# Performance work log

Measured on AMD Instinct MI355X. Metric: run time of the kernel, lower is better.

Reference implementation:

```python
import jax, jax.numpy as jnp
import numpy as np

N_NODES = 100_000
N_EDGES = 1_600_000
N_FEAT = 64
E_FEAT = 32
OUT_FEAT = 64


def _xavier_normal(key, shape, gain):
    fan_out, fan_in = shape
    std = gain * np.sqrt(2.0 / (fan_in + fan_out))
    return jax.random.normal(key, shape, dtype=jnp.float32) * std


def setup_inputs() -> dict:
    key = jax.random.key(0)
    ks = jax.random.split(key, 9)
    d_cat = 2 * N_FEAT + E_FEAT  # 160
    n_feat = jax.random.normal(ks[0], (N_NODES, N_FEAT), dtype=jnp.float32)
    e_feat = jax.random.normal(ks[1], (N_EDGES, E_FEAT), dtype=jnp.float32)
    src = jax.random.randint(ks[2], (N_EDGES,), 0, N_NODES, dtype=jnp.int32)
    dst = jax.random.randint(ks[3], (N_EDGES,), 0, N_NODES, dtype=jnp.int32)
    gain = np.sqrt(2.0)
    bound_msg = 1.0 / np.sqrt(d_cat)
    return {
        "n_feat": n_feat,
        "e_feat": e_feat,
        "src": src,
        "dst": dst,
        # W_msg uses default torch Linear init (kaiming-uniform-ish); exact init irrelevant for correctness
        "W_msg_w": jax.random.uniform(ks[4], (OUT_FEAT, d_cat), jnp.float32, -bound_msg, bound_msg),
        "W_msg_b": jax.random.uniform(ks[5], (OUT_FEAT,), jnp.float32, -bound_msg, bound_msg),
        # W uses xavier_normal with gain sqrt(2)
        "W_w": _xavier_normal(ks[6], (2 * OUT_FEAT, d_cat), gain),
        "W_b": jax.random.uniform(ks[7], (2 * OUT_FEAT,), jnp.float32, -bound_msg, bound_msg),
        "a": _xavier_normal(ks[8], (2 * OUT_FEAT, 1), gain),
    }


def reference(n_feat, e_feat, src, dst, W_msg_w, W_msg_b, W_w, W_b, a):
    # gather: per-edge concat [E, 2*n_feat + e_feat]
    feat_cat = jnp.concatenate([n_feat[src], n_feat[dst], e_feat], axis=1)
    # edge attention logits: leaky_relu((feat_cat @ W^T + b) @ a)  -> [E]
    w_feat = feat_cat @ W_w.T + W_b                      # [E, 2*out_feat]
    logits = jax.nn.leaky_relu(w_feat @ a[:, 0])         # [E]
    # edge softmax grouped by destination node
    seg_max = jax.ops.segment_max(logits, dst, num_segments=N_NODES)  # [N]
    ex = jnp.exp(logits - seg_max[dst])                  # [E]
    seg_sum = jax.ops.segment_sum(ex, dst, num_segments=N_NODES)     # [N]
    att = ex / seg_sum[dst]                              # [E]
    # messages and weighted scatter-sum aggregation
    msg = feat_cat @ W_msg_w.T + W_msg_b                 # [E, out_feat]
    agg = jax.ops.segment_sum(att[:, None] * msg, dst, num_segments=N_NODES)  # [N, out_feat]
    return jax.nn.relu(agg)
```

## Files before the change

kernel.cpp:

```cpp
#include <hip/hip_runtime.h>
#include <hip/hip_bf16.h>
#include <hip/hip_fp16.h>

#define N_NODES 100000
#define N_EDGES 1600000
#define NF 64
#define EF 32

#define SCAN_B 512
#define SCAN_NB ((N_NODES + SCAN_B - 1) / SCAN_B)


__device__ __forceinline__ unsigned pkh2(float a, float b) {
  __half2 h = __floats2half2_rn(a, b);
  return *reinterpret_cast<unsigned*>(&h);
}

__global__ __launch_bounds__(256) void k0_prep(
    const float* __restrict__ Ww, const float* __restrict__ Wb,
    const float* __restrict__ a, const float* __restrict__ Wmsg,
    float* __restrict__ v, float* __restrict__ W1T, float* __restrict__ W2T,
    float* __restrict__ WmeT) {
  int t = threadIdx.x;
  for (int j = t; j < 160; j += 256) {
    float s = 0.f;
    for (int k = 0; k < 128; ++k) s = fmaf(a[k], Ww[k * 160 + j], s);
    v[j] = s;
  }
  if (t == 0) {
    float s = 0.f;
    for (int k = 0; k < 128; ++k) s = fmaf(a[k], Wb[k], s);
    v[160] = s;
  }
  for (int idx = t; idx < 64 * 64; idx += 256) {
    int j = idx >> 6, i = idx & 63;
    W1T[idx] = Wmsg[i * 160 + j];
    W2T[idx] = Wmsg[i * 160 + 64 + j];
  }
  for (int idx = t; idx < 32 * 64; idx += 256) {
    int j = idx >> 6, i = idx & 63;
    WmeT[idx] = Wmsg[i * 160 + 128 + j];
  }
}

__global__ __launch_bounds__(256) void k1_node(
    const float* __restrict__ nf_g, const float* __restrict__ v,
    const float* __restrict__ W1T, const float* __restrict__ W2T,
    float* __restrict__ s1, float* __restrict__ s2,
    __half* __restrict__ m_src_h, float* __restrict__ m_dst) {
  int n = blockIdx.x * 256 + threadIdx.x;
  if (n >= N_NODES) return;
  const float4* nf4 = (const float4*)(nf_g + (size_t)n * NF);
  float acc[64];
#pragma unroll
  for (int i = 0; i < 64; ++i) acc[i] = 0.f;
  float s1a = 0.f, s2a = 0.f;
  for (int j4 = 0; j4 < 16; ++j4) {
    float4 q = nf4[j4];
    float xs[4] = {q.x, q.y, q.z, q.w};
#pragma unroll
    for (int u = 0; u < 4; ++u) {
      int j = j4 * 4 + u;
      float x = xs[u];
      s1a = fmaf(v[j], x, s1a);
      s2a = fmaf(v[64 + j], x, s2a);
      const float* w = W1T + j * 64;
#pragma unroll
      for (int i = 0; i < 64; ++i) acc[i] = fmaf(w[i], x, acc[i]);
    }
  }
  s1[n] = s1a;
  s2[n] = s2a;
  uint4* ms4 = (uint4*)(m_src_h + (size_t)n * NF);
#pragma unroll
  for (int b = 0; b < 8; ++b)
    ms4[b] = make_uint4(pkh2(acc[b * 8 + 0], acc[b * 8 + 1]),
                        pkh2(acc[b * 8 + 2], acc[b * 8 + 3]),
                        pkh2(acc[b * 8 + 4], acc[b * 8 + 5]),
                        pkh2(acc[b * 8 + 6], acc[b * 8 + 7]));
#pragma unroll
  for (int i = 0; i < 64; ++i) acc[i] = 0.f;
  for (int j4 = 0; j4 < 16; ++j4) {
    float4 q = nf4[j4];
    float xs[4] = {q.x, q.y, q.z, q.w};
#pragma unroll
    for (int u = 0; u < 4; ++u) {
      int j = j4 * 4 + u;
      float x = xs[u];
      const float* w = W2T + j * 64;
#pragma unroll
      for (int i = 0; i < 64; ++i) acc[i] = fmaf(w[i], x, acc[i]);
    }
  }
  float* md = m_dst + (size_t)n * NF;
#pragma unroll
  for (int i = 0; i < 64; ++i) md[i] = acc[i];
}

__global__ __launch_bounds__(256) void k_count(const int* __restrict__ dst,
                                               int* __restrict__ cnt) {
  int e = blockIdx.x * 256 + threadIdx.x;
  if (e < N_EDGES) atomicAdd(&cnt[dst[e]], 1);
}

__global__ __launch_bounds__(SCAN_B) void kS1(const int* __restrict__ cnt,
                                              int* __restrict__ bsum) {
  __shared__ int sh[SCAN_B];
  int t = threadIdx.x;
  int i = blockIdx.x * SCAN_B + t;
  sh[t] = (i < N_NODES) ? cnt[i] : 0;
  __syncthreads();
  for (int d = SCAN_B / 2; d > 0; d >>= 1) {
    if (t < d) sh[t] += sh[t + d];
    __syncthreads();
  }
  if (t == 0) bsum[blockIdx.x] = sh[0];
}

__global__ __launch_bounds__(256) void kS2(const int* __restrict__ bsum,
                                           int* __restrict__ boff,
                                           int* __restrict__ row_ptr) {
  __shared__ int sh[256];
  int t = threadIdx.x;
  sh[t] = (t < SCAN_NB) ? bsum[t] : 0;
  __syncthreads();
  for (int d = 1; d < 256; d <<= 1) {
    int val = (t >= d) ? sh[t - d] : 0;
    __syncthreads();
    sh[t] += val;
    __syncthreads();
  }
  if (t < SCAN_NB) boff[t] = (t == 0) ? 0 : sh[t - 1];
  if (t == 255) row_ptr[N_NODES] = sh[255];
}

__global__ __launch_bounds__(SCAN_B) void kS3(const int* __restrict__ cnt,
                                              const int* __restrict__ boff,
                                              int* __restrict__ row_ptr,
                                              int* __restrict__ cursor) {
  __shared__ int sh[SCAN_B];
  int t = threadIdx.x;
  int i = blockIdx.x * SCAN_B + t;
  int val = (i < N_NODES) ? cnt[i] : 0;
  sh[t] = val;
  __syncthreads();
  for (int d = 1; d < SCAN_B; d <<= 1) {
    int u = (t >= d) ? sh[t - d] : 0;
    __syncthreads();
    sh[t] += u;
    __syncthreads();
  }
  if (i < N_NODES) {
    int excl = boff[blockIdx.x] + sh[t] - val;
    row_ptr[i] = excl;
    cursor[i] = excl;
  }
}

__global__ __launch_bounds__(256) void kE_scatter(
    const int* __restrict__ src, const int* __restrict__ dst,
    const float* __restrict__ e_feat, const float* __restrict__ s1,
    const float* __restrict__ s2, const float* __restrict__ v,
    int* __restrict__ cursor, unsigned long long* __restrict__ edata,
    __half* __restrict__ ef_s) {
  int e = blockIdx.x * 256 + threadIdx.x;
  if (e >= N_EDGES) return;
  int sn = src[e], dn = dst[e];
  const float4* efr = (const float4*)(e_feat + (size_t)e * EF);
  float4 q[8];
#pragma unroll
  for (int i = 0; i < 8; ++i) q[i] = efr[i];
  float t = 0.f;
#pragma unroll
  for (int i = 0; i < 8; ++i) {
    t = fmaf(q[i].x, v[128 + i * 4 + 0], t);
    t = fmaf(q[i].y, v[128 + i * 4 + 1], t);
    t = fmaf(q[i].z, v[128 + i * 4 + 2], t);
    t = fmaf(q[i].w, v[128 + i * 4 + 3], t);
  }
  float lg = s1[sn] + s2[dn] + t + v[160];
  float l = lg > 0.f ? lg : 0.01f * lg;
  float ex = __expf(l);
  int p = atomicAdd(&cursor[dn], 1);
  edata[p] = ((unsigned long long)(unsigned)sn << 32) |
             (unsigned long long)__float_as_uint(ex);
  uint4* o4 = (uint4*)(ef_s + (size_t)p * EF);
#pragma unroll
  for (int i = 0; i < 4; ++i)
    o4[i] = make_uint4(pkh2(q[2 * i].x, q[2 * i].y),
                       pkh2(q[2 * i].z, q[2 * i].w),
                       pkh2(q[2 * i + 1].x, q[2 * i + 1].y),
                       pkh2(q[2 * i + 1].z, q[2 * i + 1].w));
}

__global__ __launch_bounds__(256) void k3_agg(
    const int* __restrict__ row_ptr, const int2* __restrict__ edata,
    const __half* __restrict__ ef_s, const __half* __restrict__ m_src_h,
    const float* __restrict__ m_dst, const float* __restrict__ WmeT,
    const float* __restrict__ Wmsg_b, float* __restrict__ out) {
  int lane = threadIdx.x & 63;
  int wid = threadIdx.x >> 6;
  int n = blockIdx.x * 4 + wid;
  if (n >= N_NODES) return;
  int start = row_ptr[n];
  int end = row_ptr[n + 1];
  int g = lane >> 4;
  int c2 = lane & 15;
  float sum_ex = 0.f, acc_ms = 0.f;
  float aefx = 0.f, aefy = 0.f;
  for (int base = start; base < end; base += 64) {
    int2 md = make_int2(0, 0);
    if (base + lane < end) md = edata[base + lane];
    int m = end - base;
    if (m > 64) m = 64;
    int mm4 = (m + 3) & ~3;
    for (int k = 0; k < mm4; k += 4) {
      float ex0 = __uint_as_float((unsigned)__shfl(md.x, k + 0));
      float ex1 = __uint_as_float((unsigned)__shfl(md.x, k + 1));
      float ex2 = __uint_as_float((unsigned)__shfl(md.x, k + 2));
      float ex3 = __uint_as_float((unsigned)__shfl(md.x, k + 3));
      int s0 = __shfl(md.y, k + 0);
      int s1i = __shfl(md.y, k + 1);
      int s2i = __shfl(md.y, k + 2);
      int s3 = __shfl(md.y, k + 3);
      float exg = (g == 0) ? ex0 : (g == 1) ? ex1 : (g == 2) ? ex2 : ex3;
      const __half2* ep =
          (const __half2*)(ef_s + ((size_t)(base + k + g)) * EF + c2 * 2);
      float2 ef2 = __half22float2(*ep);
      aefx = fmaf(exg, ef2.x, aefx);
      aefy = fmaf(exg, ef2.y, aefy);
      float ms0 = __half2float(m_src_h[(size_t)s0 * NF + lane]);
      float ms1 = __half2float(m_src_h[(size_t)s1i * NF + lane]);
      float ms2 = __half2float(m_src_h[(size_t)s2i * NF + lane]);
      float ms3 = __half2float(m_src_h[(size_t)s3 * NF + lane]);
      sum_ex += (ex0 + ex1) + (ex2 + ex3);
      acc_ms = fmaf(ex0, ms0, acc_ms);
      acc_ms = fmaf(ex1, ms1, acc_ms);
      acc_ms = fmaf(ex2, ms2, acc_ms);
      acc_ms = fmaf(ex3, ms3, acc_ms);
    }
  }
  aefx += __shfl_xor(aefx, 16);
  aefx += __shfl_xor(aefx, 32);
  aefy += __shfl_xor(aefy, 16);
  aefy += __shfl_xor(aefy, 32);
  float mm = 0.f;
#pragma unroll
  for (int jp = 0; jp < 16; ++jp) {
    float ea = __shfl(aefx, jp);
    float eb = __shfl(aefy, jp);
    mm = fmaf(WmeT[(2 * jp) * 64 + lane], ea, mm);
    mm = fmaf(WmeT[(2 * jp + 1) * 64 + lane], eb, mm);
  }
  float o = 0.f;
  if (sum_ex > 0.f) {
    o = (acc_ms + mm) / sum_ex + m_dst[(size_t)n * NF + lane] + Wmsg_b[lane];
    o = fmaxf(o, 0.f);
  }
  out[(size_t)n * NF + lane] = o;
}

extern "C" void kernel_launch(void* const* d_in, const int* in_sizes, int n_in,
                              void* d_out, int out_size, void* d_ws,
                              size_t ws_size, hipStream_t stream) {
  const float* n_feat = (const float*)d_in[0];
  const float* e_feat = (const float*)d_in[1];
  const int* src = (const int*)d_in[2];
  const int* dst = (const int*)d_in[3];
  const float* Wmsg_w = (const float*)d_in[4];
  const float* Wmsg_b = (const float*)d_in[5];
  const float* W_w = (const float*)d_in[6];
  const float* W_b = (const float*)d_in[7];
  const float* a = (const float*)d_in[8];
  float* out = (float*)d_out;

  char* ws = (char*)d_ws;
  size_t off = 0;
  auto alloc = [&](size_t bytes) -> char* {
    char* p = ws + off;
    off = (off + bytes + 255) & ~(size_t)255;
    return p;
  };
  float* v = (float*)alloc(161 * 4);
  float* W1T = (float*)alloc(64 * 64 * 4);
  float* W2T = (float*)alloc(64 * 64 * 4);
  float* WmeT = (float*)alloc(32 * 64 * 4);
  float* s1 = (float*)alloc(N_NODES * 4);
  float* s2 = (float*)alloc(N_NODES * 4);
  __half* m_src_h = (__half*)alloc((size_t)N_NODES * NF * 2);
  float* m_dst = (float*)alloc((size_t)N_NODES * NF * 4);
  int* cnt = (int*)alloc(N_NODES * 4);
  int* row_ptr = (int*)alloc((N_NODES + 1) * 4);
  int* cursor = (int*)alloc(N_NODES * 4);
  int* bsum = (int*)alloc(SCAN_NB * 4);
  int* boff = (int*)alloc(SCAN_NB * 4);
  unsigned long long* edata = (unsigned long long*)alloc((size_t)N_EDGES * 8);
  __half* ef_s = (__half*)alloc(((size_t)N_EDGES + 8) * EF * 2);
  if (off > ws_size) return;

  k0_prep<<<1, 256, 0, stream>>>(W_w, W_b, a, Wmsg_w, v, W1T, W2T, WmeT);
  k1_node<<<(N_NODES + 255) / 256, 256, 0, stream>>>(n_feat, v, W1T, W2T, s1,
                                                     s2, m_src_h, m_dst);
  hipMemsetAsync(cnt, 0, N_NODES * 4, stream);
  k_count<<<(N_EDGES + 255) / 256, 256, 0, stream>>>(dst, cnt);
  kS1<<<SCAN_NB, SCAN_B, 0, stream>>>(cnt, bsum);
  kS2<<<1, 256, 0, stream>>>(bsum, boff, row_ptr);
  kS3<<<SCAN_NB, SCAN_B, 0, stream>>>(cnt, boff, row_ptr, cursor);
  kE_scatter<<<(N_EDGES + 255) / 256, 256, 0, stream>>>(src, dst, e_feat, s1,
                                                        s2, v, cursor, edata,
                                                        ef_s);
  k3_agg<<<(N_NODES + 3) / 4, 256, 0, stream>>>(row_ptr, (const int2*)edata,
                                                ef_s, m_src_h, m_dst, WmeT,
                                                Wmsg_b, out);
}
```

Baseline: 627.5 us.

## Embed source indices in fp16 edge-feature LSBs and compute logits in aggregation

The scatter kernel no longer computes attention logits or writes a separate 8-byte edge-data array. Instead it hides the 17-bit source node index in the low mantissa bits of the packed fp16 edge features. The aggregation kernel recovers the indices with ballots and recomputes the logit and exp from the fp16 features, s1, s2 and v. It also prefetches the next group of edges one iteration ahead. This removes an edge-sized write and read pass, at the cost of perturbing the feature LSBs and computing logits from reduced-precision features.

```diff
diff --git a/kernel.cpp b/kernel.cpp
--- a/kernel.cpp
+++ b/kernel.cpp
@@ -159,43 +159,38 @@
 
 __global__ __launch_bounds__(256) void kE_scatter(
     const int* __restrict__ src, const int* __restrict__ dst,
-    const float* __restrict__ e_feat, const float* __restrict__ s1,
-    const float* __restrict__ s2, const float* __restrict__ v,
-    int* __restrict__ cursor, unsigned long long* __restrict__ edata,
-    __half* __restrict__ ef_s) {
+    const float* __restrict__ e_feat, int* __restrict__ cursor,
+    uint4* __restrict__ ef_s4) {
   int e = blockIdx.x * 256 + threadIdx.x;
   if (e >= N_EDGES) return;
-  int sn = src[e], dn = dst[e];
+  unsigned sn = (unsigned)src[e];
+  int dn = dst[e];
+  int p = atomicAdd(&cursor[dn], 1);
   const float4* efr = (const float4*)(e_feat + (size_t)e * EF);
   float4 q[8];
 #pragma unroll
   for (int i = 0; i < 8; ++i) q[i] = efr[i];
-  float t = 0.f;
+  unsigned u[16];
 #pragma unroll
   for (int i = 0; i < 8; ++i) {
-    t = fmaf(q[i].x, v[128 + i * 4 + 0], t);
-    t = fmaf(q[i].y, v[128 + i * 4 + 1], t);
-    t = fmaf(q[i].z, v[128 + i * 4 + 2], t);
-    t = fmaf(q[i].w, v[128 + i * 4 + 3], t);
-  }
-  float lg = s1[sn] + s2[dn] + t + v[160];
-  float l = lg > 0.f ? lg : 0.01f * lg;
-  float ex = __expf(l);
-  int p = atomicAdd(&cursor[dn], 1);
-  edata[p] = ((unsigned long long)(unsigned)sn << 32) |
-             (unsigned long long)__float_as_uint(ex);
-  uint4* o4 = (uint4*)(ef_s + (size_t)p * EF);
-#pragma unroll
-  for (int i = 0; i < 4; ++i)
-    o4[i] = make_uint4(pkh2(q[2 * i].x, q[2 * i].y),
-                       pkh2(q[2 * i].z, q[2 * i].w),
-                       pkh2(q[2 * i + 1].x, q[2 * i + 1].y),
-                       pkh2(q[2 * i + 1].z, q[2 * i + 1].w));
+    u[2 * i] = pkh2(q[i].x, q[i].y);
+    u[2 * i + 1] = pkh2(q[i].z, q[i].w);
+  }
+#pragma unroll
+  for (int j = 0; j < 16; ++j)
+    u[j] = (u[j] & ~1u) | ((sn >> j) & 1u);
+  u[0] = (u[0] & ~0x10000u) | (((sn >> 16) & 1u) << 16);
+  uint4* o = ef_s4 + (size_t)p * 4;
+  o[0] = make_uint4(u[0], u[1], u[2], u[3]);
+  o[1] = make_uint4(u[4], u[5], u[6], u[7]);
+  o[2] = make_uint4(u[8], u[9], u[10], u[11]);
+  o[3] = make_uint4(u[12], u[13], u[14], u[15]);
 }
 
 __global__ __launch_bounds__(256) void k3_agg(
-    const int* __restrict__ row_ptr, const int2* __restrict__ edata,
-    const __half* __restrict__ ef_s, const __half* __restrict__ m_src_h,
+    const int* __restrict__ row_ptr, const unsigned* __restrict__ efu,
+    const __half* __restrict__ m_src_h, const float* __restrict__ s1,
+    const float* __restrict__ s2, const float* __restrict__ v,
     const float* __restrict__ m_dst, const float* __restrict__ WmeT,
     const float* __restrict__ Wmsg_b, float* __restrict__ out) {
   int lane = threadIdx.x & 63;
@@ -206,39 +201,55 @@
   int end = row_ptr[n + 1];
   int g = lane >> 4;
   int c2 = lane & 15;
+  float vlo = v[128 + 2 * c2];
+  float vhi = v[128 + 2 * c2 + 1];
+  float cbias = v[160];
+  float s2n = s2[n];
   float sum_ex = 0.f, acc_ms = 0.f;
   float aefx = 0.f, aefy = 0.f;
-  for (int base = start; base < end; base += 64) {
-    int2 md = make_int2(0, 0);
-    if (base + lane < end) md = edata[base + lane];
-    int m = end - base;
-    if (m > 64) m = 64;
-    int mm4 = (m + 3) & ~3;
-    for (int k = 0; k < mm4; k += 4) {
-      float ex0 = __uint_as_float((unsigned)__shfl(md.x, k + 0));
-      float ex1 = __uint_as_float((unsigned)__shfl(md.x, k + 1));
-      float ex2 = __uint_as_float((unsigned)__shfl(md.x, k + 2));
-      float ex3 = __uint_as_float((unsigned)__shfl(md.x, k + 3));
-      int s0 = __shfl(md.y, k + 0);
-      int s1i = __shfl(md.y, k + 1);
-      int s2i = __shfl(md.y, k + 2);
-      int s3 = __shfl(md.y, k + 3);
-      float exg = (g == 0) ? ex0 : (g == 1) ? ex1 : (g == 2) ? ex2 : ex3;
-      const __half2* ep =
-          (const __half2*)(ef_s + ((size_t)(base + k + g)) * EF + c2 * 2);
-      float2 ef2 = __half22float2(*ep);
-      aefx = fmaf(exg, ef2.x, aefx);
-      aefy = fmaf(exg, ef2.y, aefy);
-      float ms0 = __half2float(m_src_h[(size_t)s0 * NF + lane]);
-      float ms1 = __half2float(m_src_h[(size_t)s1i * NF + lane]);
-      float ms2 = __half2float(m_src_h[(size_t)s2i * NF + lane]);
-      float ms3 = __half2float(m_src_h[(size_t)s3 * NF + lane]);
-      sum_ex += (ex0 + ex1) + (ex2 + ex3);
-      acc_ms = fmaf(ex0, ms0, acc_ms);
-      acc_ms = fmaf(ex1, ms1, acc_ms);
-      acc_ms = fmaf(ex2, ms2, acc_ms);
-      acc_ms = fmaf(ex3, ms3, acc_ms);
-    }
+  int slot0 = start + g;
+  unsigned ucur = efu[(size_t)min(slot0, N_EDGES - 1) * 16 + c2];
+  for (int k = start; k < end; k += 4) {
+    int slotn = k + 4 + g;
+    unsigned unext = efu[(size_t)min(slotn, N_EDGES - 1) * 16 + c2];
+    unsigned long long b0 = __ballot((int)(ucur & 1u));
+    unsigned long long b1 = __ballot((int)(ucur & 0x10000u));
+    int s0 = (int)((b0 >> 0) & 0xFFFF) | ((int)((b1 >> 0) & 1) << 16);
+    int s1i = (int)((b0 >> 16) & 0xFFFF) | ((int)((b1 >> 16) & 1) << 16);
+    int s2i = (int)((b0 >> 32) & 0xFFFF) | ((int)((b1 >> 32) & 1) << 16);
+    int s3 = (int)((b0 >> 48) & 0xFFFF) | ((int)((b1 >> 48) & 1) << 16);
+    s0 = min(s0, N_NODES - 1);
+    s1i = min(s1i, N_NODES - 1);
+    s2i = min(s2i, N_NODES - 1);
+    s3 = min(s3, N_NODES - 1);
+    int sg = (g < 2) ? (g ? s1i : s0) : ((g == 2) ? s2i : s3);
+    float ms0 = __half2float(m_src_h[(size_t)s0 * NF + lane]);
+    float ms1 = __half2float(m_src_h[(size_t)s1i * NF + lane]);
+    float ms2 = __half2float(m_src_h[(size_t)s2i * NF + lane]);
+    float ms3 = __half2float(m_src_h[(size_t)s3 * NF + lane]);
+    __half2 h2 = *reinterpret_cast<__half2*>(&ucur);
+    float2 ef2 = __half22float2(h2);
+    float pt = fmaf(ef2.y, vhi, ef2.x * vlo);
+    pt += __shfl_xor(pt, 1);
+    pt += __shfl_xor(pt, 2);
+    pt += __shfl_xor(pt, 4);
+    pt += __shfl_xor(pt, 8);
+    float lg = s1[sg] + s2n + pt + cbias;
+    float l = lg > 0.f ? lg : 0.01f * lg;
+    float ex = __expf(l);
+    float exv = ((k + g) < end) ? ex : 0.f;
+    aefx = fmaf(exv, ef2.x, aefx);
+    aefy = fmaf(exv, ef2.y, aefy);
+    float ex0 = __shfl(exv, 0);
+    float ex1 = __shfl(exv, 16);
+    float ex2 = __shfl(exv, 32);
+    float ex3 = __shfl(exv, 48);
+    sum_ex += (ex0 + ex1) + (ex2 + ex3);
+    acc_ms = fmaf(ex0, ms0, acc_ms);
+    acc_ms = fmaf(ex1, ms1, acc_ms);
+    acc_ms = fmaf(ex2, ms2, acc_ms);
+    acc_ms = fmaf(ex3, ms3, acc_ms);
+    ucur = unext;
   }
   aefx += __shfl_xor(aefx, 16);
   aefx += __shfl_xor(aefx, 32);
@@ -294,7 +305,6 @@
   int* cursor = (int*)alloc(N_NODES * 4);
   int* bsum = (int*)alloc(SCAN_NB * 4);
   int* boff = (int*)alloc(SCAN_NB * 4);
-  unsigned long long* edata = (unsigned long long*)alloc((size_t)N_EDGES * 8);
   __half* ef_s = (__half*)alloc(((size_t)N_EDGES + 8) * EF * 2);
   if (off > ws_size) return;
 
@@ -306,10 +316,9 @@
   kS1<<<SCAN_NB, SCAN_B, 0, stream>>>(cnt, bsum);
   kS2<<<1, 256, 0, stream>>>(bsum, boff, row_ptr);
   kS3<<<SCAN_NB, SCAN_B, 0, stream>>>(cnt, boff, row_ptr, cursor);
-  kE_scatter<<<(N_EDGES + 255) / 256, 256, 0, stream>>>(src, dst, e_feat, s1,
-                                                        s2, v, cursor, edata,
-                                                        ef_s);
-  k3_agg<<<(N_NODES + 3) / 4, 256, 0, stream>>>(row_ptr, (const int2*)edata,
-                                                ef_s, m_src_h, m_dst, WmeT,
-                                                Wmsg_b, out);
-}
+  kE_scatter<<<(N_EDGES + 255) / 256, 256, 0, stream>>>(
+      src, dst, e_feat, cursor, (uint4*)ef_s);
+  k3_agg<<<(N_NODES + 3) / 4, 256, 0, stream>>>(
+      row_ptr, (const unsigned*)ef_s, m_src_h, s1, s2, v, m_dst, WmeT,
+      Wmsg_b, out);
+}
```

After: 609.8 us. 2.8% less time.
